# Kernel tuning notes

Measured on AMD Instinct MI355X. Metric: run time of the kernel, lower is better.

Reference implementation:

```python
import jax, jax.numpy as jnp
from jax import lax
import numpy as np

NUM_CLASSES = 80
SCORE_THR = 0.05
MIN_SIZE = 1.0
IOU_THR = 0.5
IMTOP = 100
PRE_NMS_K = 1000   # per-image candidate cap before NMS (jit-safe substitute for dynamic nonzero filtering)
N_IMG = 2
BBOX_CLIP = float(np.log(1000.0 / 16.0))  # standard dw/dh clamp in decode_boxes(clamp=True)


def setup_inputs() -> dict:
    key = jax.random.key(0)
    ks = jax.random.split(key, 12)
    R, C, S, CLIN = 2000, 256, 7, 1024
    c1 = C * S * S
    roi_maps = jax.random.normal(ks[0], (R, C, S, S), jnp.float32) * 0.1
    xy = jax.random.uniform(ks[1], (R, 2), jnp.float32, 0.0, 600.0)
    wh = jax.random.uniform(ks[2], (R, 2), jnp.float32, 8.0, 200.0)
    proposals = jnp.concatenate([xy, xy + wh], axis=-1)  # valid xyxy boxes
    imidx = jnp.sort(jax.random.randint(ks[3], (R,), 0, N_IMG)).astype(jnp.int32)
    imsizes = jnp.full((N_IMG, 2), 800.0, jnp.float32)  # (h, w) per image
    def lin(k, o, i):
        return jax.random.normal(k, (o, i), jnp.float32) * (1.0 / np.sqrt(i))
    return {
        'roi_maps': roi_maps, 'proposals': proposals, 'imidx': imidx, 'imsizes': imsizes,
        'fc1_w': lin(ks[4], CLIN, c1), 'fc1_b': jnp.zeros((CLIN,), jnp.float32),
        'fc2_w': lin(ks[5], CLIN, CLIN), 'fc2_b': jnp.zeros((CLIN,), jnp.float32),
        'cls_w': lin(ks[6], 1 + NUM_CLASSES, CLIN), 'cls_b': jnp.zeros((1 + NUM_CLASSES,), jnp.float32),
        'reg_w': lin(ks[7], NUM_CLASSES * 4, CLIN), 'reg_b': jnp.zeros((NUM_CLASSES * 4,), jnp.float32),
    }


def _nms_single(boxes, scores, cls):
    # boxes [K,4] xyxy (sorted by score desc), scores [K] (-1 = invalid), cls [K]
    K = scores.shape[0]
    valid = scores > 0.0
    # batched_nms trick: offset boxes by class so different classes never overlap
    off = cls.astype(boxes.dtype) * (jnp.max(boxes) + 1.0)
    ob = boxes + off[:, None]
    x1, y1, x2, y2 = ob[:, 0], ob[:, 1], ob[:, 2], ob[:, 3]
    area = (x2 - x1) * (y2 - y1)
    iw = jnp.clip(jnp.minimum(x2[:, None], x2[None, :]) - jnp.maximum(x1[:, None], x1[None, :]), 0.0)
    ih = jnp.clip(jnp.minimum(y2[:, None], y2[None, :]) - jnp.maximum(y1[:, None], y1[None, :]), 0.0)
    inter = iw * ih
    iou = inter / (area[:, None] + area[None, :] - inter + 1e-9)  # [K,K]
    ar = jnp.arange(K)

    def body(i, carry):
        sup, keep = carry
        k = jnp.logical_not(sup[i])
        keep = keep.at[i].set(k)
        sup = sup | (k & (iou[i] > IOU_THR) & (ar > i))
        return (sup, keep)

    sup, keep = lax.fori_loop(0, K, body, (jnp.logical_not(valid), jnp.zeros((K,), bool)))
    order = jnp.sort(jnp.where(keep, ar, K))[:IMTOP]
    vo = order < K
    idx = jnp.minimum(order, K - 1)
    b = jnp.where(vo[:, None], boxes[idx], 0.0)
    s = jnp.where(vo, scores[idx], 0.0)
    c = jnp.where(vo, cls[idx], -1)
    return b, s, c


def _forward(roi_maps, proposals, imsizes, fc1_w, fc1_b, fc2_w, fc2_b,
             cls_w, cls_b, reg_w, reg_b, imidx):
    R = roi_maps.shape[0]
    x = roi_maps.reshape(R, -1)
    x = jax.nn.relu(x @ fc1_w.T + fc1_b)
    x = jax.nn.relu(x @ fc2_w.T + fc2_b)
    reg = (x @ reg_w.T + reg_b).reshape(R, NUM_CLASSES, 4)  # per-class deltas
    logit = x @ cls_w.T + cls_b                              # [R, 1+C]
    scr = jax.nn.softmax(logit, axis=-1)[:, :-1]             # bckg_class_first=False -> drop last
    # convert_to_cwh
    pw = proposals[:, 2] - proposals[:, 0]
    ph = proposals[:, 3] - proposals[:, 1]
    pcx = proposals[:, 0] + 0.5 * pw
    pcy = proposals[:, 1] + 0.5 * ph
    # decode_boxes, mults=(0.1, 0.2), clamp dw/dh
    dx = reg[..., 0] * 0.1
    dy = reg[..., 1] * 0.1
    dw = jnp.minimum(reg[..., 2] * 0.2, BBOX_CLIP)
    dh = jnp.minimum(reg[..., 3] * 0.2, BBOX_CLIP)
    cx = dx * pw[:, None] + pcx[:, None]
    cy = dy * ph[:, None] + pcy[:, None]
    w = jnp.exp(dw) * pw[:, None]
    h = jnp.exp(dh) * ph[:, None]
    boxes = jnp.stack([cx - 0.5 * w, cy - 0.5 * h, cx + 0.5 * w, cy + 0.5 * h], axis=-1)  # [R,C,4]
    # clamp_to_canvas: imsizes is (h, w)
    sz = imsizes[imidx]  # [R,2]
    maxs = jnp.stack([sz[:, 1], sz[:, 0], sz[:, 1], sz[:, 0]], axis=-1)[:, None, :]
    boxes = jnp.clip(boxes, 0.0, maxs)
    bw = boxes[..., 2] - boxes[..., 0]
    bh = boxes[..., 3] - boxes[..., 1]
    # score_thr filter + remove_small, expressed as score masking (jit-safe)
    mask = (scr > SCORE_THR) & (bw >= MIN_SIZE) & (bh >= MIN_SIZE)
    scores = jnp.where(mask, scr, -1.0)  # [R,C]
    flat_boxes = boxes.reshape(-1, 4)
    flat_cls = jnp.broadcast_to(jnp.arange(NUM_CLASSES), (R, NUM_CLASSES)).reshape(-1)
    # per-image candidate scores, pre-NMS top-K
    img_mask = imidx[None, :] == jnp.arange(N_IMG)[:, None]            # [N,R]
    img_scores = jnp.where(img_mask[:, :, None], scores[None], -1.0).reshape(N_IMG, -1)
    top_s, top_i = lax.top_k(img_scores, PRE_NMS_K)                    # [N,K]
    b_k = flat_boxes[top_i]                                            # [N,K,4]
    c_k = flat_cls[top_i]                                              # [N,K]
    return jax.vmap(_nms_single)(b_k, top_s, c_k)


def reference(roi_maps, proposals, imidx, imsizes, fc1_w, fc1_b, fc2_w, fc2_b,
              cls_w, cls_b, reg_w, reg_b):
    return _forward(roi_maps, proposals, imsizes, fc1_w, fc1_b, fc2_w, fc2_b,
                    cls_w, cls_b, reg_w, reg_b, imidx)
```

## Files before the change

### kernel.cpp

```cpp
#include <hip/hip_runtime.h>
#include <cstdint>

typedef unsigned int u32;
typedef unsigned long long u64;
typedef _Float16 f16;
typedef f16 f16x8 __attribute__((ext_vector_type(8)));
typedef f16 f16x4 __attribute__((ext_vector_type(4)));
typedef float f32x4 __attribute__((ext_vector_type(4)));

#define R_ROIS 2000
#define CIN 12544
#define HID 1024
#define NCLS 80
#define NHEAD 401
#define RC (R_ROIS*NCLS)
#define KTOP 1000
#define IMTOP 100
#define KEY_NEG1 0x407FFFFFu
#define BBOX_CLIPV 4.135166556742356f
#define NCHUNK 157

__device__ __forceinline__ u32 fkey(float f) {
  u32 u = __float_as_uint(f);
  return (u & 0x80000000u) ? ~u : (u | 0x80000000u);
}
__device__ __forceinline__ float fkeyinv(u32 k) {
  u32 b = (k & 0x80000000u) ? (k & 0x7FFFFFFFu) : ~k;
  return __uint_as_float(b);
}
__device__ __forceinline__ u32 mkey(const u32* keys, const int* imidx, int i, int g) {
  int r = i / NCLS;
  return (imidx[r] == g) ? keys[i] : KEY_NEG1;
}

__device__ __forceinline__ void lds16(const f16* gsrc, f16* ldst) {
  __builtin_amdgcn_global_load_lds(
      (const __attribute__((address_space(1))) void*)gsrc,
      (__attribute__((address_space(3))) void*)ldst, 16, 0, 0);
}

__global__ __launch_bounds__(512, 4)
void gemm_f16x3(const f16* __restrict__ A1, const f16* __restrict__ A2,
                const f16* __restrict__ B1, const f16* __restrict__ B2,
                float* __restrict__ C, int M, int N, int K, int kLen)
{
  __shared__ __align__(16) f16 As1[2][128 * 32];
  __shared__ __align__(16) f16 As2[2][128 * 32];
  __shared__ __align__(16) f16 Bs1[2][128 * 32];
  __shared__ __align__(16) f16 Bs2[2][128 * 32];

  int gx = gridDim.x, gy = gridDim.y;
  int nblk = gx * gy * gridDim.z;
  int lid = blockIdx.x + gx * (blockIdx.y + gy * blockIdx.z);
  int cpx = nblk >> 3;
  int nlid = (lid & 7) * cpx + (lid >> 3);
  int bx = nlid % gx;
  int rem = nlid / gx;
  int by = rem % gy;
  int bz = rem / gy;

  int t = threadIdx.x;
  int w = t >> 6, lane = t & 63;
  int wm = w >> 2, wn = w & 3;
  int m0 = by * 128, n0 = bx * 128;
  int k0 = bz * kLen;
// ... 58 lines not shown
#pragma unroll
    for (int mi = 0; mi < 4; ++mi)
#pragma unroll
      for (int ni = 0; ni < 2; ++ni) {
        acc[mi][ni] = __builtin_amdgcn_mfma_f32_16x16x32_f16(af1[mi], bf1[ni], acc[mi][ni], 0, 0, 0);
        acc[mi][ni] = __builtin_amdgcn_mfma_f32_16x16x32_f16(af1[mi], bf2[ni], acc[mi][ni], 0, 0, 0);
        acc[mi][ni] = __builtin_amdgcn_mfma_f32_16x16x32_f16(af2[mi], bf1[ni], acc[mi][ni], 0, 0, 0);
      }
    __builtin_amdgcn_s_setprio(0);
    __builtin_amdgcn_sched_barrier(0);
    asm volatile("s_waitcnt vmcnt(0)" ::: "memory");
    __builtin_amdgcn_s_barrier();
    __builtin_amdgcn_sched_barrier(0);
    cur ^= 1;
  }

  int crow = m0 + wm * 64 + (lane >> 4) * 4;
  int ccol = n0 + wn * 32 + (lane & 15);
#pragma unroll
  for (int mi = 0; mi < 4; ++mi)
#pragma unroll
    for (int r = 0; r < 4; ++r) {
      int rm = crow + mi * 16 + r;
      if (rm < M) {
#pragma unroll
        for (int ni = 0; ni < 2; ++ni) {
          int cc = ccol + ni * 16;
          if (cc < N) atomicAdd(&C[(size_t)rm * N + cc], acc[mi][ni][r]);
        }
      }
    }
}

__global__ void split3_k(const float* __restrict__ s0, int c0,
                         const float* __restrict__ s1, int c1,
                         const float* __restrict__ s2, int c2,
                         f16* __restrict__ d0a, f16* __restrict__ d0b,
                         f16* __restrict__ d1a, f16* __restrict__ d1b,
                         f16* __restrict__ d2a, f16* __restrict__ d2b)
{
  int total = c0 + c1 + c2;
  for (int i = blockIdx.x * blockDim.x + threadIdx.x; i < total; i += gridDim.x * blockDim.x) {
    const float* src; f16 *da, *db; int j;
    if (i < c0) { src = s0; da = d0a; db = d0b; j = i; }
    else if (i < c0 + c1) { src = s1; da = d1a; db = d1b; j = i - c0; }
    else { src = s2; da = d2a; db = d2b; j = i - c0 - c1; }
    float4 v = ((const float4*)src)[j];
    f16x4 o1, o2;
    o1[0] = (f16)v.x; o2[0] = (f16)(v.x - (float)o1[0]);
    o1[1] = (f16)v.y; o2[1] = (f16)(v.y - (float)o1[1]);
    o1[2] = (f16)v.z; o2[2] = (f16)(v.z - (float)o1[2]);
    o1[3] = (f16)v.w; o2[3] = (f16)(v.w - (float)o1[3]);
    ((f16x4*)da)[j] = o1;
    ((f16x4*)db)[j] = o2;
  }
}

__global__ void packhead_k(const float* __restrict__ clsw, const float* __restrict__ regw,
                           f16* __restrict__ W1, f16* __restrict__ W2)
{
  int i = blockIdx.x * blockDim.x + threadIdx.x;
  if (i >= 512 * 256) return;
  int r = i >> 8, c4 = i & 255;
  int rr = (r < NHEAD) ? r : (NHEAD - 1);
  const float* src = (rr < 81) ? (clsw + (size_t)rr * HID) : (regw + (size_t)(rr - 81) * HID);
  float4 v = ((const float4*)src)[c4];
  f16x4 o1, o2;
  o1[0] = (f16)v.x; o2[0] = (f16)(v.x - (float)o1[0]);
  o1[1] = (f16)v.y; o2[1] = (f16)(v.y - (float)o1[1]);
  o1[2] = (f16)v.z; o2[2] = (f16)(v.z - (float)o1[2]);
  o1[3] = (f16)v.w; o2[3] = (f16)(v.w - (float)o1[3]);
  ((f16x4*)W1)[i] = o1;
  ((f16x4*)W2)[i] = o2;
}

__global__ void biasfill_k(const float* __restrict__ clsb, const float* __restrict__ regb,
                           float* __restrict__ H)
{
  int i = blockIdx.x * blockDim.x + threadIdx.x;
  if (i >= R_ROIS * NHEAD) return;
  int c = i % NHEAD;
  H[i] = (c < 81) ? clsb[c] : regb[c - 81];
}

__global__ void bias_relu_split_k(const float* __restrict__ X, const float* __restrict__ bias,
                                  f16* __restrict__ H1, f16* __restrict__ H2, int total)
{
  int i = blockIdx.x * blockDim.x + threadIdx.x;
  if (i >= total) return;
  float v = fmaxf(X[i] + bias[i & (HID - 1)], 0.f);
  f16 a = (f16)v;
  H1[i] = a;
  H2[i] = (f16)(v - (float)a);
}

__global__ __launch_bounds__(256, 2)
void gemm128(const float* __restrict__ A, int lda,
             const float* __restrict__ B, int ldb,
             float* __restrict__ C, int M, int N, int kLen)
{
  __shared__ float As[128][20];
  __shared__ float Bs[128][20];
  int t = threadIdx.x;
  int tx = t & 15, ty = t >> 4;
  int m0 = blockIdx.y * 128, n0 = blockIdx.x * 128;
  int k0 = blockIdx.z * kLen;
  float acc[8][8];
#pragma unroll
  for (int i = 0; i < 8; ++i)
#pragma unroll
    for (int j = 0; j < 8; ++j) acc[i][j] = 0.f;

  int lr = t >> 2;
  int lk = (t & 3) * 4;

  for (int ks = 0; ks < kLen; ks += 16) {
#pragma unroll
    for (int p = 0; p < 2; ++p) {
      int row = lr + p * 64;
      int rm = m0 + row; if (rm > M - 1) rm = M - 1;
      float4 av = *(const float4*)(A + (size_t)rm * lda + k0 + ks + lk);
      *(float4*)&As[row][lk] = av;
      int rn = n0 + row; if (rn > N - 1) rn = N - 1;
      float4 bv = *(const float4*)(B + (size_t)rn * ldb + k0 + ks + lk);
      *(float4*)&Bs[row][lk] = bv;
    }
    __syncthreads();
#pragma unroll
    for (int kk = 0; kk < 16; kk += 4) {
      float4 a4[8], b4[8];
#pragma unroll
      for (int i = 0; i < 8; ++i) a4[i] = *(const float4*)&As[ty + (i << 4)][kk];
#pragma unroll
      for (int j = 0; j < 8; ++j) b4[j] = *(const float4*)&Bs[tx + (j << 4)][kk];
#pragma unroll
      for (int i = 0; i < 8; ++i)
#pragma unroll
        for (int j = 0; j < 8; ++j) {
          acc[i][j] += a4[i].x * b4[j].x;
          acc[i][j] += a4[i].y * b4[j].y;
          acc[i][j] += a4[i].z * b4[j].z;
          acc[i][j] += a4[i].w * b4[j].w;
        }
    }
    __syncthreads();
  }
#pragma unroll
  for (int i = 0; i < 8; ++i) {
    int rm = m0 + ty + (i << 4);
    if (rm < M) {
#pragma unroll
      for (int j = 0; j < 8; ++j) {
        int rn = n0 + tx + (j << 4);
        atomicAdd(&C[(size_t)rm * N + rn], acc[i][j]);
      }
    }
  }
}

__global__ void bias_relu_k(float* __restrict__ X, const float* __restrict__ bias, int total4)
{
  int i4 = blockIdx.x * blockDim.x + threadIdx.x;
  if (i4 >= total4) return;
  int c4 = i4 & 255;
  float4 v = ((float4*)X)[i4];
  float4 b = ((const float4*)bias)[c4];
  v.x = fmaxf(v.x + b.x, 0.f);
  v.y = fmaxf(v.y + b.y, 0.f);
  v.z = fmaxf(v.z + b.z, 0.f);
  v.w = fmaxf(v.w + b.w, 0.f);
  ((float4*)X)[i4] = v;
}

__global__ __launch_bounds__(256)
void gemm_heads(const float* __restrict__ A,
                const float* __restrict__ clsw, const float* __restrict__ clsb,
                const float* __restrict__ regw, const float* __restrict__ regb,
                float* __restrict__ H)
{
  __shared__ float As[64][36];
  __shared__ float Bs[64][36];
  int t = threadIdx.x;
  int tx = t & 15, ty = t >> 4;
  int m0 = blockIdx.y * 64, n0 = blockIdx.x * 64;
  float acc[4][4] = {};
  int lr = t >> 3;
  int lk = (t & 7) * 4;

  for (int ks = 0; ks < HID; ks += 32) {
#pragma unroll
    for (int p = 0; p < 2; ++p) {
      int row = lr + p * 32;
      int rm = m0 + row; if (rm > R_ROIS - 1) rm = R_ROIS - 1;
      *(float4*)&As[row][lk] = *(const float4*)(A + (size_t)rm * HID + ks + lk);
      int rn = n0 + row; if (rn > NHEAD - 1) rn = NHEAD - 1;
      const float* bp = (rn < 81) ? (clsw + (size_t)rn * HID) : (regw + (size_t)(rn - 81) * HID);
      *(float4*)&Bs[row][lk] = *(const float4*)(bp + ks + lk);
    }
    __syncthreads();
#pragma unroll
    for (int kk = 0; kk < 32; kk += 4) {
      float4 a4[4], b4[4];
#pragma unroll
      for (int i = 0; i < 4; ++i) a4[i] = *(const float4*)&As[ty + (i << 4)][kk];
#pragma unroll
      for (int j = 0; j < 4; ++j) b4[j] = *(const float4*)&Bs[tx + (j << 4)][kk];
#pragma unroll
      for (int i = 0; i < 4; ++i)
#pragma unroll
        for (int j = 0; j < 4; ++j) {
          acc[i][j] += a4[i].x * b4[j].x;
          acc[i][j] += a4[i].y * b4[j].y;
          acc[i][j] += a4[i].z * b4[j].z;
          acc[i][j] += a4[i].w * b4[j].w;
        }
    }
    __syncthreads();
  }
#pragma unroll
  for (int i = 0; i < 4; ++i) {
    int rm = m0 + ty + (i << 4);
#pragma unroll
    for (int j = 0; j < 4; ++j) {
      int rn = n0 + tx + (j << 4);
      if (rm < R_ROIS && rn < NHEAD) {
        float b = (rn < 81) ? clsb[rn] : regb[rn - 81];
        H[(size_t)rm * NHEAD + rn] = acc[i][j] + b;
      }
    }
  }
}

__global__ __launch_bounds__(256)
void decode_k(const float* __restrict__ H, const float* __restrict__ prop,
              const int* __restrict__ imidx, const float* __restrict__ imsz,
              u32* __restrict__ keys, float* __restrict__ boxes)
{
  int lane = threadIdx.x & 63;
  int r = blockIdx.x * 4 + (threadIdx.x >> 6);
  const float* h = H + (size_t)r * NHEAD;
  float l0 = h[lane];
  float l1 = (lane < 17) ? h[64 + lane] : -1e30f;
  float mx = fmaxf(l0, l1);
#pragma unroll
  for (int o = 32; o; o >>= 1) mx = fmaxf(mx, __shfl_xor(mx, o));
  float e0 = expf(l0 - mx);
  float e1 = (lane < 17) ? expf(l1 - mx) : 0.f;
  float s = e0 + e1;
#pragma unroll
  for (int o = 32; o; o >>= 1) s += __shfl_xor(s, o);

  float px1 = prop[r * 4 + 0], py1 = prop[r * 4 + 1];
  float px2 = prop[r * 4 + 2], py2 = prop[r * 4 + 3];
  float pw = px2 - px1, ph = py2 - py1;
  float pcx = px1 + 0.5f * pw, pcy = py1 + 0.5f * ph;
  int g = imidx[r];
  float imh = imsz[g * 2 + 0], imw = imsz[g * 2 + 1];

#pragma unroll
  for (int q = 0; q < 2; ++q) {
    int c = (q == 0) ? lane : 64 + lane;
    bool on = (q == 0) ? true : (lane < 16);
    if (on) {
      float e = (q == 0) ? e0 : e1;
      float scr = e / s;
      const float* rg = h + 81 + c * 4;
      float dx = rg[0] * 0.1f, dy = rg[1] * 0.1f;
      float dw = fminf(rg[2] * 0.2f, BBOX_CLIPV);
      float dh = fminf(rg[3] * 0.2f, BBOX_CLIPV);
      float cx = dx * pw + pcx, cy = dy * ph + pcy;
      float w = expf(dw) * pw, hh = expf(dh) * ph;
      float x1 = cx - 0.5f * w, y1 = cy - 0.5f * hh;
      float x2 = cx + 0.5f * w, y2 = cy + 0.5f * hh;
      x1 = fminf(fmaxf(x1, 0.f), imw);
      x2 = fminf(fmaxf(x2, 0.f), imw);
      y1 = fminf(fmaxf(y1, 0.f), imh);
      y2 = fminf(fmaxf(y2, 0.f), imh);
      float bw = x2 - x1, bh = y2 - y1;
      bool msk = (scr > 0.05f) && (bw >= 1.f) && (bh >= 1.f);
      float sm = msk ? scr : -1.f;
      int idx = r * 80 + c;
      keys[idx] = fkey(sm);
      ((float4*)boxes)[idx] = make_float4(x1, y1, x2, y2);
    }
  }
}

__global__ void hist_k(const u32* __restrict__ keys, const int* __restrict__ imidx,
                       const u32* __restrict__ sel, u32* __restrict__ hist, int level, int nbins)
{
  __shared__ u32 lh[2048];
  int t = threadIdx.x, g = blockIdx.y;
  for (int b = t; b < 2048; b += 256) lh[b] = 0;
  __syncthreads();
  u32 b1 = 0, pre21 = 0;
  if (level == 2) b1 = sel[g * 8 + 0];
  if (level == 3) pre21 = (sel[g * 8 + 0] << 11) | sel[g * 8 + 1];
  for (int i = blockIdx.x * 256 + t; i < RC; i += gridDim.x * 256) {
    u32 k = mkey(keys, imidx, i, g);
    if (level == 1) atomicAdd(&lh[k >> 21], 1u);
    else if (level == 2) { if ((k >> 21) == b1) atomicAdd(&lh[(k >> 10) & 0x7FFu], 1u); }
    else { if ((k >> 10) == pre21) atomicAdd(&lh[k & 0x3FFu], 1u); }
  }
  __syncthreads();
  for (int b = t; b < nbins; b += 256) { u32 v = lh[b]; if (v) atomicAdd(&hist[g * nbins + b], v); }
}

__global__ void find_k(const u32* __restrict__ hist, int nbins, u32* __restrict__ sel, int level)
{
  __shared__ u32 sh[256];
  int t = threadIdx.x, g = blockIdx.x;
  int per = nbins >> 8;
  const u32* h = hist + g * nbins;
  u32 mySum = 0;
  for (int jj = 0; jj < per; ++jj) mySum += h[t * per + jj];
  u32 base = (level == 1) ? 0u : sel[g * 8 + 3];
  sh[t] = mySum; __syncthreads();
  for (int off = 1; off < 256; off <<= 1) {
    u32 v = (t + off < 256) ? sh[t + off] : 0u; __syncthreads();
    sh[t] += v; __syncthreads();
  }
  u32 c = base + ((t < 255) ? sh[t + 1] : 0u);
  for (int jj = per - 1; jj >= 0; --jj) {
    int b = t * per + jj;
    u32 cnt = h[b];
    if (c < KTOP && c + cnt >= KTOP) {
      if (level == 1) { sel[g * 8 + 0] = (u32)b; sel[g * 8 + 3] = c; }
      else if (level == 2) { sel[g * 8 + 1] = (u32)b; sel[g * 8 + 3] = c; }
      else {
        u32 T = (sel[g * 8 + 0] << 21) | (sel[g * 8 + 1] << 10) | (u32)b;
        sel[g * 8 + 4] = T; sel[g * 8 + 3] = c; sel[g * 8 + 5] = KTOP - c;
      }
    }
    c += cnt;
  }
}

__global__ void eqcount_k(const u32* __restrict__ keys, const int* __restrict__ imidx,
                          const u32* __restrict__ sel, u32* __restrict__ eqcnt)
{
  int g = blockIdx.y, t = threadIdx.x;
  int i = blockIdx.x * 1024 + t;
  u32 T = sel[g * 8 + 4];
  bool eq = (i < RC) && (mkey(keys, imidx, i, g) == T);
  u64 bal = __ballot(eq);
  __shared__ u32 wc[16];
  if ((t & 63) == 0) wc[t >> 6] = (u32)__popcll(bal);
  __syncthreads();
  if (t == 0) {
    u32 sum = 0;
    for (int w = 0; w < 16; ++w) sum += wc[w];
    eqcnt[g * 160 + blockIdx.x] = sum;
  }
}

__global__ void eqscan_k(const u32* __restrict__ eqcnt, u32* __restrict__ eqoff)
{
  __shared__ u32 sh[256];
  int t = threadIdx.x, g = blockIdx.x;
  u32 v = (t < NCHUNK) ? eqcnt[g * 160 + t] : 0u;
  sh[t] = v; __syncthreads();
  for (int off = 1; off < 256; off <<= 1) {
    u32 u = (t >= off) ? sh[t - off] : 0u; __syncthreads();
    sh[t] += u; __syncthreads();
  }
  if (t < NCHUNK) eqoff[g * 160 + t] = sh[t] - v;
}

__global__ void emit_k(const u32* __restrict__ keys, const int* __restrict__ imidx,
                       const u32* __restrict__ sel, const u32* __restrict__ eqoff,
                       u32* __restrict__ cntgt, u32* __restrict__ cand)
{
  int g = blockIdx.y, t = threadIdx.x;
  int i = blockIdx.x * 1024 + t;
  u32 T = sel[g * 8 + 4], m = sel[g * 8 + 5], ra = sel[g * 8 + 3];
  u32 k = (i < RC) ? mkey(keys, imidx, i, g) : 0u;
  if (k > T) { u32 p = atomicAdd(&cntgt[g], 1u); cand[g * 1024 + p] = (u32)i; }
  bool eq = (k == T);
  u64 bal = __ballot(eq);
  int w = t >> 6, lane = t & 63;
  __shared__ u32 wc[16];
  if (lane == 0) wc[w] = (u32)__popcll(bal);
  __syncthreads();
  u32 wb = 0;
  for (int x = 0; x < w; ++x) wb += wc[x];
  if (eq) {
    u32 lanePre = (u32)__popcll(bal & ((1ull << lane) - 1ull));
    u32 rank = eqoff[g * 160 + blockIdx.x] + wb + lanePre;
    if (rank < m) cand[g * 1024 + ra + rank] = (u32)i;
  }
}

__global__ __launch_bounds__(512)
void sort_k(const u32* __restrict__ cand, const u32* __restrict__ keys,
            const int* __restrict__ imidx, u64* __restrict__ sorted)
{
  __shared__ u64 sm[1024];
  int t = threadIdx.x, g = blockIdx.x;
#pragma unroll
  for (int p = 0; p < 2; ++p) {
    int s = t + p * 512;
    u64 e = ~0ull;
    if (s < KTOP) {
      u32 i = cand[g * 1024 + s];
      u32 k = mkey(keys, imidx, (int)i, g);
      e = ((u64)(~k) << 32) | (u64)i;
    }
    sm[s] = e;
  }
  __syncthreads();
  for (int kk = 2; kk <= 1024; kk <<= 1)
    for (int j = kk >> 1; j > 0; j >>= 1) {
#pragma unroll
      for (int p = 0; p < 2; ++p) {
        int i = t + p * 512;
        int ixj = i ^ j;
        if (ixj > i) {
          u64 a = sm[i], b = sm[ixj];
          bool up = ((i & kk) == 0);
          if ((a > b) == up) { sm[i] = b; sm[ixj] = a; }
        }
      }
      __syncthreads();
    }
  sorted[g * 1024 + t] = sm[t];
  sorted[g * 1024 + t + 512] = sm[t + 512];
}

__global__ void gather_k(const u64* __restrict__ sorted, const float* __restrict__ boxes,
                         u32* __restrict__ idx_k, float* __restrict__ sc_k,
                         float4* __restrict__ box_k, u64* __restrict__ inval,
                         float4* __restrict__ ob, float* __restrict__ area)
{
  __shared__ u32 smax;
  int t = threadIdx.x, g = blockIdx.x;
  if (t == 0) smax = 0;
  __syncthreads();
  u64 e = sorted[g * 1024 + t];
  u32 idx = (u32)e;
  u32 k = ~(u32)(e >> 32);
  float sc = fkeyinv(k);
  bool val = (t < KTOP) && (sc > 0.f);
  float4 b = make_float4(0.f, 0.f, 0.f, 0.f);
  if (t < KTOP) {
    idx_k[g * 1024 + t] = idx;
    sc_k[g * 1024 + t] = sc;
    b = ((const float4*)boxes)[idx];
    box_k[g * 1024 + t] = b;
    u32 m1 = __float_as_uint(b.x) > __float_as_uint(b.y) ? __float_as_uint(b.x) : __float_as_uint(b.y);
    u32 m2 = __float_as_uint(b.z) > __float_as_uint(b.w) ? __float_as_uint(b.z) : __float_as_uint(b.w);
    atomicMax(&smax, m1 > m2 ? m1 : m2);
  }
  u64 bal = __ballot(!val);
  if ((t & 63) == 0) inval[g * 16 + (t >> 6)] = bal;
  __syncthreads();
  float mx = __uint_as_float(smax);
  if (t < KTOP) {
    float off = (float)(idx % NCLS) * (mx + 1.0f);
    float4 o = make_float4(b.x + off, b.y + off, b.z + off, b.w + off);
    ob[g * 1024 + t] = o;
    area[g * 1024 + t] = (o.z - o.x) * (o.w - o.y);
  }
}

__global__ __launch_bounds__(256)
void nmsmat_k(const float4* __restrict__ ob, const float* __restrict__ area, u64* __restrict__ Mrow)
{
  __shared__ float4 sob[KTOP];
  __shared__ float sar[KTOP];
  int t = threadIdx.x, g = blockIdx.y;
  for (int s = t; s < KTOP; s += 256) { sob[s] = ob[g * 1024 + s]; sar[s] = area[g * 1024 + s]; }
  __syncthreads();
  int w = blockIdx.x * 256 + t;
  if (w >= KTOP * 16) return;
  int i = w >> 4, jw = w & 15;
  float4 bi = sob[i];
  float ai = sar[i];
  u64 bits = 0;
  int jbase = jw * 64;
  for (int b = 0; b < 64; ++b) {
    int j = jbase + b;
    if (j < KTOP && j > i) {
      float4 bj = sob[j];
      float iw = fminf(bi.z, bj.z) - fmaxf(bi.x, bj.x); iw = fmaxf(iw, 0.f);
      float ih = fminf(bi.w, bj.w) - fmaxf(bi.y, bj.y); ih = fmaxf(ih, 0.f);
      float inter = iw * ih;
      float iou = inter / (ai + sar[j] - inter + 1e-9f);
// ... 32 lines not shown
      sc = sc_k[g * 1024 + i];
      cf = (float)(idx_k[g * 1024 + i] % NCLS);
    }
    ((float4*)out)[g * IMTOP + s] = b;
    out[800 + g * IMTOP + s] = sc;
    out[1000 + g * IMTOP + s] = cf;
  }
}

extern "C" void kernel_launch(void* const* d_in, const int* in_sizes, int n_in,
                              void* d_out, int out_size, void* d_ws, size_t ws_size,
                              hipStream_t stream) {
  (void)in_sizes; (void)n_in; (void)out_size;
  const float* roi  = (const float*)d_in[0];
  const float* prop = (const float*)d_in[1];
  const int*   imix = (const int*)d_in[2];
  const float* imsz = (const float*)d_in[3];
  const float* fc1w = (const float*)d_in[4];
  const float* fc1b = (const float*)d_in[5];
  const float* fc2w = (const float*)d_in[6];
  const float* fc2b = (const float*)d_in[7];
  const float* clsw = (const float*)d_in[8];
  const float* clsb = (const float*)d_in[9];
  const float* regw = (const float*)d_in[10];
  const float* regb = (const float*)d_in[11];
  float* out = (float*)d_out;

  char* ws = (char*)d_ws;
  size_t o = 0;
  auto alloc = [&](size_t bytes) { size_t r = o; o += (bytes + 255) & ~(size_t)255; return r; };
  float* C1    = (float*)(ws + alloc((size_t)R_ROIS * HID * 4));
  float* C2    = (float*)(ws + alloc((size_t)R_ROIS * HID * 4));
  float* HEADS = (float*)(ws + alloc((size_t)R_ROIS * NHEAD * 4));
  u32*   KEYS  = (u32*)  (ws + alloc((size_t)RC * 4));
  float* BOXES = (float*)(ws + alloc((size_t)RC * 16));
  u64*   MROW  = (u64*)  (ws + alloc((size_t)2 * KTOP * 16 * 8));
  u64*   SORTED= (u64*)  (ws + alloc(2 * 1024 * 8));
  u32*   CAND  = (u32*)  (ws + alloc(2 * 1024 * 4));
  u32*   IDXK  = (u32*)  (ws + alloc(2 * 1024 * 4));
  float* SCK   = (float*)(ws + alloc(2 * 1024 * 4));
  float4* BOXK = (float4*)(ws + alloc(2 * 1024 * 16));
  float4* OBK  = (float4*)(ws + alloc(2 * 1024 * 16));
  float* AREA  = (float*)(ws + alloc(2 * 1024 * 4));
  u64*   INVAL = (u64*)  (ws + alloc(2 * 16 * 8));
  size_t zz0 = o;
  u32* HIST1 = (u32*)(ws + alloc(2 * 2048 * 4));
  u32* HIST2 = (u32*)(ws + alloc(2 * 2048 * 4));
  u32* HIST3 = (u32*)(ws + alloc(2 * 1024 * 4));
  u32* SEL   = (u32*)(ws + alloc(2 * 8 * 4));
  u32* CNTGT = (u32*)(ws + alloc(2 * 4));
  size_t zzBytes = o - zz0;
  u32* EQCNT = (u32*)(ws + alloc(2 * 160 * 4));
  u32* EQOFF = (u32*)(ws + alloc(2 * 160 * 4));

  f16* A1h = (f16*)(ws + alloc((size_t)R_ROIS * CIN * 2));
  f16* A2h = (f16*)(ws + alloc((size_t)R_ROIS * CIN * 2));
  f16* B1h = (f16*)(ws + alloc((size_t)HID * CIN * 2));
  f16* B2h = (f16*)(ws + alloc((size_t)HID * CIN * 2));
  f16* X1h = (f16*)(ws + alloc((size_t)R_ROIS * HID * 2));
  f16* X2h = (f16*)(ws + alloc((size_t)R_ROIS * HID * 2));
  f16* W1h = (f16*)(ws + alloc((size_t)HID * HID * 2));
  f16* W2h = (f16*)(ws + alloc((size_t)HID * HID * 2));
  f16* Y1h = (f16*)(ws + alloc((size_t)R_ROIS * HID * 2));
  f16* Y2h = (f16*)(ws + alloc((size_t)R_ROIS * HID * 2));
  f16* WH1 = (f16*)(ws + alloc((size_t)512 * HID * 2));
  f16* WH2 = (f16*)(ws + alloc((size_t)512 * HID * 2));
  bool fp16ok = (o <= ws_size);

  hipMemsetAsync(C1, 0, (size_t)2 * R_ROIS * HID * 4, stream);
  hipMemsetAsync(ws + zz0, 0, zzBytes, stream);

  if (fp16ok) {
    split3_k<<<2048, 256, 0, stream>>>(roi, R_ROIS * CIN / 4, fc1w, HID * CIN / 4,
                                       fc2w, HID * HID / 4,
                                       A1h, A2h, B1h, B2h, W1h, W2h);
    packhead_k<<<512, 256, 0, stream>>>(clsw, regw, WH1, WH2);
    biasfill_k<<<(R_ROIS * NHEAD + 255) / 256, 256, 0, stream>>>(clsb, regb, HEADS);
    gemm_f16x3<<<dim3(8, 16, 4), 512, 0, stream>>>(A1h, A2h, B1h, B2h, C1, R_ROIS, HID, CIN, 3136);
    bias_relu_split_k<<<(R_ROIS * HID + 255) / 256, 256, 0, stream>>>(C1, fc1b, X1h, X2h, R_ROIS * HID);
    gemm_f16x3<<<dim3(8, 16, 4), 512, 0, stream>>>(X1h, X2h, W1h, W2h, C2, R_ROIS, HID, HID, 256);
    bias_relu_split_k<<<(R_ROIS * HID + 255) / 256, 256, 0, stream>>>(C2, fc2b, Y1h, Y2h, R_ROIS * HID);
    gemm_f16x3<<<dim3(4, 16, 4), 512, 0, stream>>>(Y1h, Y2h, WH1, WH2, HEADS, R_ROIS, NHEAD, HID, 256);
  } else {
    gemm128<<<dim3(8, 16, 4), 256, 0, stream>>>(roi, CIN, fc1w, CIN, C1, R_ROIS, HID, 3136);
    bias_relu_k<<<2000, 256, 0, stream>>>(C1, fc1b, R_ROIS * HID / 4);
    gemm128<<<dim3(8, 16, 4), 256, 0, stream>>>(C1, HID, fc2w, HID, C2, R_ROIS, HID, 256);
    bias_relu_k<<<2000, 256, 0, stream>>>(C2, fc2b, R_ROIS * HID / 4);
    gemm_heads<<<dim3(7, 32), 256, 0, stream>>>(C2, clsw, clsb, regw, regb, HEADS);
  }
  decode_k<<<500, 256, 0, stream>>>(HEADS, prop, imix, imsz, KEYS, BOXES);
  hist_k<<<dim3(128, 2), 256, 0, stream>>>(KEYS, imix, SEL, HIST1, 1, 2048);
  find_k<<<2, 256, 0, stream>>>(HIST1, 2048, SEL, 1);
  hist_k<<<dim3(128, 2), 256, 0, stream>>>(KEYS, imix, SEL, HIST2, 2, 2048);
  find_k<<<2, 256, 0, stream>>>(HIST2, 2048, SEL, 2);
  hist_k<<<dim3(128, 2), 256, 0, stream>>>(KEYS, imix, SEL, HIST3, 3, 1024);
  find_k<<<2, 256, 0, stream>>>(HIST3, 1024, SEL, 3);
  eqcount_k<<<dim3(NCHUNK, 2), 1024, 0, stream>>>(KEYS, imix, SEL, EQCNT);
  eqscan_k<<<2, 256, 0, stream>>>(EQCNT, EQOFF);
  emit_k<<<dim3(NCHUNK, 2), 1024, 0, stream>>>(KEYS, imix, SEL, EQOFF, CNTGT, CAND);
  sort_k<<<2, 512, 0, stream>>>(CAND, KEYS, imix, SORTED);
  gather_k<<<2, 1024, 0, stream>>>(SORTED, BOXES, IDXK, SCK, BOXK, INVAL, OBK, AREA);
  nmsmat_k<<<dim3(63, 2), 256, 0, stream>>>(OBK, AREA, MROW);
  nmsscan_k<<<2, 64, 0, stream>>>(MROW, INVAL, IDXK, SCK, BOXK, out);
}
```

Baseline: 634.0 us.

## Fuse top-k selection pipeline into single per-image kernel and merge prep kernels

Replaces the chain of histogram, find, eqcount, scan, emit, sort and gather kernels with one select_k block per image. That block runs the three radix passes, candidate emission and the bitonic sort in shared memory, and decode now writes per-image key arrays. The three preprocessing kernels are merged into one prep_k, and bias_relu_split is vectorised to float4. This removes about a dozen small launches and a memset, but the selection now runs on only two blocks, each scanning 160K keys three times, so per-block serial work grows.

```diff
diff --git a/kernel.cpp b/kernel.cpp
--- a/kernel.cpp
+++ b/kernel.cpp
@@ -18,7 +18,6 @@
 #define IMTOP 100
 #define KEY_NEG1 0x407FFFFFu
 #define BBOX_CLIPV 4.135166556742356f
-#define NCHUNK 157
 
 __device__ __forceinline__ u32 fkey(float f) {
   u32 u = __float_as_uint(f);
@@ -27,10 +26,6 @@
 __device__ __forceinline__ float fkeyinv(u32 k) {
   u32 b = (k & 0x80000000u) ? (k & 0x7FFFFFFFu) : ~k;
   return __uint_as_float(b);
-}
-__device__ __forceinline__ u32 mkey(const u32* keys, const int* imidx, int i, int g) {
-  int r = i / NCLS;
-  return (imidx[r] == g) ? keys[i] : KEY_NEG1;
 }
 
 __device__ __forceinline__ void lds16(const f16* gsrc, f16* ldst) {
@@ -155,66 +150,70 @@
     }
 }
 
-__global__ void split3_k(const float* __restrict__ s0, int c0,
-                         const float* __restrict__ s1, int c1,
-                         const float* __restrict__ s2, int c2,
-                         f16* __restrict__ d0a, f16* __restrict__ d0b,
-                         f16* __restrict__ d1a, f16* __restrict__ d1b,
-                         f16* __restrict__ d2a, f16* __restrict__ d2b)
-{
-  int total = c0 + c1 + c2;
-  for (int i = blockIdx.x * blockDim.x + threadIdx.x; i < total; i += gridDim.x * blockDim.x) {
-    const float* src; f16 *da, *db; int j;
-    if (i < c0) { src = s0; da = d0a; db = d0b; j = i; }
-    else if (i < c0 + c1) { src = s1; da = d1a; db = d1b; j = i - c0; }
-    else { src = s2; da = d2a; db = d2b; j = i - c0 - c1; }
-    float4 v = ((const float4*)src)[j];
-    f16x4 o1, o2;
-    o1[0] = (f16)v.x; o2[0] = (f16)(v.x - (float)o1[0]);
-    o1[1] = (f16)v.y; o2[1] = (f16)(v.y - (float)o1[1]);
-    o1[2] = (f16)v.z; o2[2] = (f16)(v.z - (float)o1[2]);
-    o1[3] = (f16)v.w; o2[3] = (f16)(v.w - (float)o1[3]);
-    ((f16x4*)da)[j] = o1;
-    ((f16x4*)db)[j] = o2;
-  }
-}
-
-__global__ void packhead_k(const float* __restrict__ clsw, const float* __restrict__ regw,
-                           f16* __restrict__ W1, f16* __restrict__ W2)
-{
-  int i = blockIdx.x * blockDim.x + threadIdx.x;
-  if (i >= 512 * 256) return;
-  int r = i >> 8, c4 = i & 255;
-  int rr = (r < NHEAD) ? r : (NHEAD - 1);
-  const float* src = (rr < 81) ? (clsw + (size_t)rr * HID) : (regw + (size_t)(rr - 81) * HID);
-  float4 v = ((const float4*)src)[c4];
-  f16x4 o1, o2;
+__device__ __forceinline__ void split4(float4 v, f16x4& o1, f16x4& o2) {
   o1[0] = (f16)v.x; o2[0] = (f16)(v.x - (float)o1[0]);
   o1[1] = (f16)v.y; o2[1] = (f16)(v.y - (float)o1[1]);
   o1[2] = (f16)v.z; o2[2] = (f16)(v.z - (float)o1[2]);
   o1[3] = (f16)v.w; o2[3] = (f16)(v.w - (float)o1[3]);
-  ((f16x4*)W1)[i] = o1;
-  ((f16x4*)W2)[i] = o2;
-}
-
-__global__ void biasfill_k(const float* __restrict__ clsb, const float* __restrict__ regb,
-                           float* __restrict__ H)
-{
-  int i = blockIdx.x * blockDim.x + threadIdx.x;
-  if (i >= R_ROIS * NHEAD) return;
-  int c = i % NHEAD;
-  H[i] = (c < 81) ? clsb[c] : regb[c - 81];
+}
+
+__global__ void prep_k(const float* __restrict__ roi, const float* __restrict__ fc1w,
+                       const float* __restrict__ fc2w, const float* __restrict__ clsw,
+                       const float* __restrict__ regw, const float* __restrict__ clsb,
+                       const float* __restrict__ regb,
+                       f16* __restrict__ A1h, f16* __restrict__ A2h,
+                       f16* __restrict__ B1h, f16* __restrict__ B2h,
+                       f16* __restrict__ W1h, f16* __restrict__ W2h,
+                       f16* __restrict__ WH1, f16* __restrict__ WH2,
+                       float* __restrict__ HEADS)
+{
+  const int c0 = R_ROIS * CIN / 4;
+  const int c1 = HID * CIN / 4;
+  const int c2 = HID * HID / 4;
+  const int c3 = 512 * 256;
+  const int c4 = R_ROIS * NHEAD;
+  const int e0 = c0, e1 = e0 + c1, e2 = e1 + c2, e3 = e2 + c3, e4 = e3 + c4;
+  for (int i = blockIdx.x * blockDim.x + threadIdx.x; i < e4; i += gridDim.x * blockDim.x) {
+    f16x4 o1, o2;
+    if (i < e0) {
+      split4(((const float4*)roi)[i], o1, o2);
+      ((f16x4*)A1h)[i] = o1; ((f16x4*)A2h)[i] = o2;
+    } else if (i < e1) {
+      int j = i - e0;
+      split4(((const float4*)fc1w)[j], o1, o2);
+      ((f16x4*)B1h)[j] = o1; ((f16x4*)B2h)[j] = o2;
+    } else if (i < e2) {
+      int j = i - e1;
+      split4(((const float4*)fc2w)[j], o1, o2);
+      ((f16x4*)W1h)[j] = o1; ((f16x4*)W2h)[j] = o2;
+    } else if (i < e3) {
+      int j = i - e2;
+      int r = j >> 8, c4i = j & 255;
+      int rr = (r < NHEAD) ? r : (NHEAD - 1);
+      const float* src = (rr < 81) ? (clsw + (size_t)rr * HID) : (regw + (size_t)(rr - 81) * HID);
+      split4(((const float4*)src)[c4i], o1, o2);
+      ((f16x4*)WH1)[j] = o1; ((f16x4*)WH2)[j] = o2;
+    } else {
+      int j = i - e3;
+      int c = j % NHEAD;
+      HEADS[j] = (c < 81) ? clsb[c] : regb[c - 81];
+    }
+  }
 }
 
 __global__ void bias_relu_split_k(const float* __restrict__ X, const float* __restrict__ bias,
-                                  f16* __restrict__ H1, f16* __restrict__ H2, int total)
-{
-  int i = blockIdx.x * blockDim.x + threadIdx.x;
-  if (i >= total) return;
-  float v = fmaxf(X[i] + bias[i & (HID - 1)], 0.f);
-  f16 a = (f16)v;
-  H1[i] = a;
-  H2[i] = (f16)(v - (float)a);
+                                  f16* __restrict__ H1, f16* __restrict__ H2, int total4)
+{
+  int i4 = blockIdx.x * blockDim.x + threadIdx.x;
+  if (i4 >= total4) return;
+  float4 v = ((const float4*)X)[i4];
+  float4 b = ((const float4*)bias)[i4 & 255];
+  v.x = fmaxf(v.x + b.x, 0.f); v.y = fmaxf(v.y + b.y, 0.f);
+  v.z = fmaxf(v.z + b.z, 0.f); v.w = fmaxf(v.w + b.w, 0.f);
+  f16x4 o1, o2;
+  split4(v, o1, o2);
+  ((f16x4*)H1)[i4] = o1;
+  ((f16x4*)H2)[i4] = o2;
 }
 
 __global__ __launch_bounds__(256, 2)
@@ -233,20 +232,16 @@
   for (int i = 0; i < 8; ++i)
 #pragma unroll
     for (int j = 0; j < 8; ++j) acc[i][j] = 0.f;
-
   int lr = t >> 2;
   int lk = (t & 3) * 4;
-
   for (int ks = 0; ks < kLen; ks += 16) {
 #pragma unroll
     for (int p = 0; p < 2; ++p) {
       int row = lr + p * 64;
       int rm = m0 + row; if (rm > M - 1) rm = M - 1;
-      float4 av = *(const float4*)(A + (size_t)rm * lda + k0 + ks + lk);
-      *(float4*)&As[row][lk] = av;
+      *(float4*)&As[row][lk] = *(const float4*)(A + (size_t)rm * lda + k0 + ks + lk);
       int rn = n0 + row; if (rn > N - 1) rn = N - 1;
-      float4 bv = *(const float4*)(B + (size_t)rn * ldb + k0 + ks + lk);
-      *(float4*)&Bs[row][lk] = bv;
+      *(float4*)&Bs[row][lk] = *(const float4*)(B + (size_t)rn * ldb + k0 + ks + lk);
     }
     __syncthreads();
 #pragma unroll
@@ -273,10 +268,8 @@
     int rm = m0 + ty + (i << 4);
     if (rm < M) {
 #pragma unroll
-      for (int j = 0; j < 8; ++j) {
-        int rn = n0 + tx + (j << 4);
-        atomicAdd(&C[(size_t)rm * N + rn], acc[i][j]);
-      }
+      for (int j = 0; j < 8; ++j)
+        atomicAdd(&C[(size_t)rm * N + n0 + tx + (j << 4)], acc[i][j]);
     }
   }
 }
@@ -285,13 +278,10 @@
 {
   int i4 = blockIdx.x * blockDim.x + threadIdx.x;
   if (i4 >= total4) return;
-  int c4 = i4 & 255;
   float4 v = ((float4*)X)[i4];
-  float4 b = ((const float4*)bias)[c4];
-  v.x = fmaxf(v.x + b.x, 0.f);
-  v.y = fmaxf(v.y + b.y, 0.f);
-  v.z = fmaxf(v.z + b.z, 0.f);
-  v.w = fmaxf(v.w + b.w, 0.f);
+  float4 b = ((const float4*)bias)[i4 & 255];
+  v.x = fmaxf(v.x + b.x, 0.f); v.y = fmaxf(v.y + b.y, 0.f);
+  v.z = fmaxf(v.z + b.z, 0.f); v.w = fmaxf(v.w + b.w, 0.f);
   ((float4*)X)[i4] = v;
 }
 
@@ -309,7 +299,6 @@
   float acc[4][4] = {};
   int lr = t >> 3;
   int lk = (t & 7) * 4;
-
   for (int ks = 0; ks < HID; ks += 32) {
 #pragma unroll
     for (int p = 0; p < 2; ++p) {
@@ -357,7 +346,7 @@
 __global__ __launch_bounds__(256)
 void decode_k(const float* __restrict__ H, const float* __restrict__ prop,
               const int* __restrict__ imidx, const float* __restrict__ imsz,
-              u32* __restrict__ keys, float* __restrict__ boxes)
+              u32* __restrict__ keys0, u32* __restrict__ keys1, float* __restrict__ boxes)
 {
   int lane = threadIdx.x & 63;
   int r = blockIdx.x * 4 + (threadIdx.x >> 6);
@@ -401,168 +390,155 @@
       y2 = fminf(fmaxf(y2, 0.f), imh);
       float bw = x2 - x1, bh = y2 - y1;
       bool msk = (scr > 0.05f) && (bw >= 1.f) && (bh >= 1.f);
-      float sm = msk ? scr : -1.f;
+      u32 kk = fkey(msk ? scr : -1.f);
       int idx = r * 80 + c;
-      keys[idx] = fkey(sm);
+      keys0[idx] = (g == 0) ? kk : KEY_NEG1;
+      keys1[idx] = (g == 1) ? kk : KEY_NEG1;
       ((float4*)boxes)[idx] = make_float4(x1, y1, x2, y2);
     }
   }
 }
 
-__global__ void hist_k(const u32* __restrict__ keys, const int* __restrict__ imidx,
-                       const u32* __restrict__ sel, u32* __restrict__ hist, int level, int nbins)
+__global__ __launch_bounds__(1024)
+void select_k(const u32* __restrict__ keys0, const u32* __restrict__ keys1,
+              const float* __restrict__ boxes,
+              u32* __restrict__ idx_k, float* __restrict__ sc_k,
+              float4* __restrict__ box_k, u64* __restrict__ inval,
+              float4* __restrict__ ob, float* __restrict__ area)
 {
   __shared__ u32 lh[2048];
-  int t = threadIdx.x, g = blockIdx.y;
-  for (int b = t; b < 2048; b += 256) lh[b] = 0;
-  __syncthreads();
-  u32 b1 = 0, pre21 = 0;
-  if (level == 2) b1 = sel[g * 8 + 0];
-  if (level == 3) pre21 = (sel[g * 8 + 0] << 11) | sel[g * 8 + 1];
-  for (int i = blockIdx.x * 256 + t; i < RC; i += gridDim.x * 256) {
-    u32 k = mkey(keys, imidx, i, g);
-    if (level == 1) atomicAdd(&lh[k >> 21], 1u);
-    else if (level == 2) { if ((k >> 21) == b1) atomicAdd(&lh[(k >> 10) & 0x7FFu], 1u); }
-    else { if ((k >> 10) == pre21) atomicAdd(&lh[k & 0x3FFu], 1u); }
-  }
-  __syncthreads();
-  for (int b = t; b < nbins; b += 256) { u32 v = lh[b]; if (v) atomicAdd(&hist[g * nbins + b], v); }
-}
-
-__global__ void find_k(const u32* __restrict__ hist, int nbins, u32* __restrict__ sel, int level)
-{
-  __shared__ u32 sh[256];
-  int t = threadIdx.x, g = blockIdx.x;
-  int per = nbins >> 8;
-  const u32* h = hist + g * nbins;
-  u32 mySum = 0;
-  for (int jj = 0; jj < per; ++jj) mySum += h[t * per + jj];
-  u32 base = (level == 1) ? 0u : sel[g * 8 + 3];
-  sh[t] = mySum; __syncthreads();
-  for (int off = 1; off < 256; off <<= 1) {
-    u32 v = (t + off < 256) ? sh[t + off] : 0u; __syncthreads();
-    sh[t] += v; __syncthreads();
-  }
-  u32 c = base + ((t < 255) ? sh[t + 1] : 0u);
-  for (int jj = per - 1; jj >= 0; --jj) {
-    int b = t * per + jj;
-    u32 cnt = h[b];
+  __shared__ u32 sh[1024];
+  __shared__ u32 candL[1024];
+  __shared__ u64 sm[1024];
+  __shared__ u32 selS[8];
+  __shared__ u32 wc[16];
+  __shared__ u32 gtCnt, eqBase, smax;
+
+  int g = blockIdx.x, t = threadIdx.x;
+  int w = t >> 6, lane = t & 63;
+  const u32* keys = g ? keys1 : keys0;
+
+  lh[t] = 0; lh[t + 1024] = 0;
+  __syncthreads();
+  for (int i = t; i < RC; i += 1024) atomicAdd(&lh[keys[i] >> 21], 1u);
+  __syncthreads();
+  {
+    sh[t] = lh[2 * t] + lh[2 * t + 1];
+    __syncthreads();
+    for (int off = 1; off < 1024; off <<= 1) {
+      u32 v = (t + off < 1024) ? sh[t + off] : 0u; __syncthreads();
+      sh[t] += v; __syncthreads();
+    }
+    u32 c = (t < 1023) ? sh[t + 1] : 0u;
+    for (int jj = 1; jj >= 0; --jj) {
+      int b = 2 * t + jj;
+      u32 cnt = lh[b];
+      if (c < KTOP && c + cnt >= KTOP) { selS[0] = (u32)b; selS[2] = c; }
+      c += cnt;
+    }
+  }
+  __syncthreads();
+  u32 b1 = selS[0];
+  lh[t] = 0; lh[t + 1024] = 0;
+  __syncthreads();
+  for (int i = t; i < RC; i += 1024) {
+    u32 k = keys[i];
+    if ((k >> 21) == b1) atomicAdd(&lh[(k >> 10) & 0x7FFu], 1u);
+  }
+  __syncthreads();
+  {
+    u32 base = selS[2];
+    sh[t] = lh[2 * t] + lh[2 * t + 1];
+    __syncthreads();
+    for (int off = 1; off < 1024; off <<= 1) {
+      u32 v = (t + off < 1024) ? sh[t + off] : 0u; __syncthreads();
+      sh[t] += v; __syncthreads();
+    }
+    u32 c = base + ((t < 1023) ? sh[t + 1] : 0u);
+    for (int jj = 1; jj >= 0; --jj) {
+      int b = 2 * t + jj;
+      u32 cnt = lh[b];
+      if (c < KTOP && c + cnt >= KTOP) { selS[1] = (u32)b; selS[3] = c; }
+      c += cnt;
+    }
+  }
+  __syncthreads();
+  u32 pre21 = (b1 << 11) | selS[1];
+  lh[t] = 0;
+  __syncthreads();
+  for (int i = t; i < RC; i += 1024) {
+    u32 k = keys[i];
+    if ((k >> 10) == pre21) atomicAdd(&lh[k & 0x3FFu], 1u);
+  }
+  __syncthreads();
+  {
+    u32 base = selS[3];
+    sh[t] = lh[t];
+    __syncthreads();
+    for (int off = 1; off < 1024; off <<= 1) {
+      u32 v = (t + off < 1024) ? sh[t + off] : 0u; __syncthreads();
+      sh[t] += v; __syncthreads();
+    }
+    u32 c = base + ((t < 1023) ? sh[t + 1] : 0u);
+    u32 cnt = lh[t];
     if (c < KTOP && c + cnt >= KTOP) {
-      if (level == 1) { sel[g * 8 + 0] = (u32)b; sel[g * 8 + 3] = c; }
-      else if (level == 2) { sel[g * 8 + 1] = (u32)b; sel[g * 8 + 3] = c; }
-      else {
-        u32 T = (sel[g * 8 + 0] << 21) | (sel[g * 8 + 1] << 10) | (u32)b;
-        sel[g * 8 + 4] = T; sel[g * 8 + 3] = c; sel[g * 8 + 5] = KTOP - c;
-      }
-    }
-    c += cnt;
-  }
-}
-
-__global__ void eqcount_k(const u32* __restrict__ keys, const int* __restrict__ imidx,
-                          const u32* __restrict__ sel, u32* __restrict__ eqcnt)
-{
-  int g = blockIdx.y, t = threadIdx.x;
-  int i = blockIdx.x * 1024 + t;
-  u32 T = sel[g * 8 + 4];
-  bool eq = (i < RC) && (mkey(keys, imidx, i, g) == T);
-  u64 bal = __ballot(eq);
-  __shared__ u32 wc[16];
-  if ((t & 63) == 0) wc[t >> 6] = (u32)__popcll(bal);
-  __syncthreads();
-  if (t == 0) {
-    u32 sum = 0;
-    for (int w = 0; w < 16; ++w) sum += wc[w];
-    eqcnt[g * 160 + blockIdx.x] = sum;
-  }
-}
-
-__global__ void eqscan_k(const u32* __restrict__ eqcnt, u32* __restrict__ eqoff)
-{
-  __shared__ u32 sh[256];
-  int t = threadIdx.x, g = blockIdx.x;
-  u32 v = (t < NCHUNK) ? eqcnt[g * 160 + t] : 0u;
-  sh[t] = v; __syncthreads();
-  for (int off = 1; off < 256; off <<= 1) {
-    u32 u = (t >= off) ? sh[t - off] : 0u; __syncthreads();
-    sh[t] += u; __syncthreads();
-  }
-  if (t < NCHUNK) eqoff[g * 160 + t] = sh[t] - v;
-}
-
-__global__ void emit_k(const u32* __restrict__ keys, const int* __restrict__ imidx,
-                       const u32* __restrict__ sel, const u32* __restrict__ eqoff,
-                       u32* __restrict__ cntgt, u32* __restrict__ cand)
-{
-  int g = blockIdx.y, t = threadIdx.x;
-  int i = blockIdx.x * 1024 + t;
-  u32 T = sel[g * 8 + 4], m = sel[g * 8 + 5], ra = sel[g * 8 + 3];
-  u32 k = (i < RC) ? mkey(keys, imidx, i, g) : 0u;
-  if (k > T) { u32 p = atomicAdd(&cntgt[g], 1u); cand[g * 1024 + p] = (u32)i; }
-  bool eq = (k == T);
-  u64 bal = __ballot(eq);
-  int w = t >> 6, lane = t & 63;
-  __shared__ u32 wc[16];
-  if (lane == 0) wc[w] = (u32)__popcll(bal);
-  __syncthreads();
-  u32 wb = 0;
-  for (int x = 0; x < w; ++x) wb += wc[x];
-  if (eq) {
-    u32 lanePre = (u32)__popcll(bal & ((1ull << lane) - 1ull));
-    u32 rank = eqoff[g * 160 + blockIdx.x] + wb + lanePre;
-    if (rank < m) cand[g * 1024 + ra + rank] = (u32)i;
-  }
-}
-
-__global__ __launch_bounds__(512)
-void sort_k(const u32* __restrict__ cand, const u32* __restrict__ keys,
-            const int* __restrict__ imidx, u64* __restrict__ sorted)
-{
-  __shared__ u64 sm[1024];
-  int t = threadIdx.x, g = blockIdx.x;
-#pragma unroll
-  for (int p = 0; p < 2; ++p) {
-    int s = t + p * 512;
+      selS[4] = (pre21 << 10) | (u32)t;
+      selS[6] = c;
+      selS[5] = KTOP - c;
+    }
+  }
+  __syncthreads();
+  u32 T = selS[4], mm = selS[5], cGT = selS[6];
+
+  if (t == 0) { gtCnt = 0; eqBase = 0; }
+  __syncthreads();
+  for (int c0 = 0; c0 < RC; c0 += 1024) {
+    int i = c0 + t;
+    bool inr = (i < RC);
+    u32 k = inr ? keys[i] : 0u;
+    if (inr && k > T) { u32 p = atomicAdd(&gtCnt, 1u); candL[p] = (u32)i; }
+    bool eq = inr && (k == T);
+    u64 bal = __ballot(eq);
+    if (lane == 0) wc[w] = (u32)__popcll(bal);
+    __syncthreads();
+    u32 pre = 0, tot = 0;
+#pragma unroll
+    for (int x = 0; x < 16; ++x) { u32 v = wc[x]; if (x < w) pre += v; tot += v; }
+    if (eq) {
+      u32 rank = eqBase + pre + (u32)__popcll(bal & ((1ull << lane) - 1ull));
+      if (rank < mm) candL[cGT + rank] = (u32)i;
+    }
+    __syncthreads();
+    if (t == 0) eqBase += tot;
+    __syncthreads();
+  }
+
+  {
     u64 e = ~0ull;
-    if (s < KTOP) {
-      u32 i = cand[g * 1024 + s];
-      u32 k = mkey(keys, imidx, (int)i, g);
-      e = ((u64)(~k) << 32) | (u64)i;
-    }
-    sm[s] = e;
-  }
-  __syncthreads();
-  for (int kk = 2; kk <= 1024; kk <<= 1)
-    for (int j = kk >> 1; j > 0; j >>= 1) {
-#pragma unroll
-      for (int p = 0; p < 2; ++p) {
-        int i = t + p * 512;
-        int ixj = i ^ j;
-        if (ixj > i) {
-          u64 a = sm[i], b = sm[ixj];
-          bool up = ((i & kk) == 0);
-          if ((a > b) == up) { sm[i] = b; sm[ixj] = a; }
-        }
+    if (t < KTOP) {
+      u32 i = candL[t];
+      e = ((u64)(~keys[i]) << 32) | (u64)i;
+    }
+    sm[t] = e;
+  }
+  __syncthreads();
+  for (int kk2 = 2; kk2 <= 1024; kk2 <<= 1)
+    for (int j = kk2 >> 1; j > 0; j >>= 1) {
+      int ixj = t ^ j;
+      if (ixj > t) {
+        u64 a = sm[t], b = sm[ixj];
+        bool up = ((t & kk2) == 0);
+        if ((a > b) == up) { sm[t] = b; sm[ixj] = a; }
       }
       __syncthreads();
     }
-  sorted[g * 1024 + t] = sm[t];
-  sorted[g * 1024 + t + 512] = sm[t + 512];
-}
-
-__global__ void gather_k(const u64* __restrict__ sorted, const float* __restrict__ boxes,
-                         u32* __restrict__ idx_k, float* __restrict__ sc_k,
-                         float4* __restrict__ box_k, u64* __restrict__ inval,
-                         float4* __restrict__ ob, float* __restrict__ area)
-{
-  __shared__ u32 smax;
-  int t = threadIdx.x, g = blockIdx.x;
+
   if (t == 0) smax = 0;
   __syncthreads();
-  u64 e = sorted[g * 1024 + t];
+  u64 e = sm[t];
   u32 idx = (u32)e;
-  u32 k = ~(u32)(e >> 32);
-  float sc = fkeyinv(k);
+  u32 k2 = ~(u32)(e >> 32);
+  float sc = fkeyinv(k2);
   bool val = (t < KTOP) && (sc > 0.f);
   float4 b = make_float4(0.f, 0.f, 0.f, 0.f);
   if (t < KTOP) {
@@ -575,7 +551,7 @@
     atomicMax(&smax, m1 > m2 ? m1 : m2);
   }
   u64 bal = __ballot(!val);
-  if ((t & 63) == 0) inval[g * 16 + (t >> 6)] = bal;
+  if (lane == 0) inval[g * 16 + w] = bal;
   __syncthreads();
   float mx = __uint_as_float(smax);
   if (t < KTOP) {
@@ -674,26 +650,16 @@
   float* C1    = (float*)(ws + alloc((size_t)R_ROIS * HID * 4));
   float* C2    = (float*)(ws + alloc((size_t)R_ROIS * HID * 4));
   float* HEADS = (float*)(ws + alloc((size_t)R_ROIS * NHEAD * 4));
-  u32*   KEYS  = (u32*)  (ws + alloc((size_t)RC * 4));
+  u32*   KEYS0 = (u32*)  (ws + alloc((size_t)RC * 4));
+  u32*   KEYS1 = (u32*)  (ws + alloc((size_t)RC * 4));
   float* BOXES = (float*)(ws + alloc((size_t)RC * 16));
   u64*   MROW  = (u64*)  (ws + alloc((size_t)2 * KTOP * 16 * 8));
-  u64*   SORTED= (u64*)  (ws + alloc(2 * 1024 * 8));
-  u32*   CAND  = (u32*)  (ws + alloc(2 * 1024 * 4));
   u32*   IDXK  = (u32*)  (ws + alloc(2 * 1024 * 4));
   float* SCK   = (float*)(ws + alloc(2 * 1024 * 4));
   float4* BOXK = (float4*)(ws + alloc(2 * 1024 * 16));
   float4* OBK  = (float4*)(ws + alloc(2 * 1024 * 16));
   float* AREA  = (float*)(ws + alloc(2 * 1024 * 4));
   u64*   INVAL = (u64*)  (ws + alloc(2 * 16 * 8));
-  size_t zz0 = o;
-  u32* HIST1 = (u32*)(ws + alloc(2 * 2048 * 4));
-  u32* HIST2 = (u32*)(ws + alloc(2 * 2048 * 4));
-  u32* HIST3 = (u32*)(ws + alloc(2 * 1024 * 4));
-  u32* SEL   = (u32*)(ws + alloc(2 * 8 * 4));
-  u32* CNTGT = (u32*)(ws + alloc(2 * 4));
-  size_t zzBytes = o - zz0;
-  u32* EQCNT = (u32*)(ws + alloc(2 * 160 * 4));
-  u32* EQOFF = (u32*)(ws + alloc(2 * 160 * 4));
 
   f16* A1h = (f16*)(ws + alloc((size_t)R_ROIS * CIN * 2));
   f16* A2h = (f16*)(ws + alloc((size_t)R_ROIS * CIN * 2));
@@ -710,18 +676,14 @@
   bool fp16ok = (o <= ws_size);
 
   hipMemsetAsync(C1, 0, (size_t)2 * R_ROIS * HID * 4, stream);
-  hipMemsetAsync(ws + zz0, 0, zzBytes, stream);
 
   if (fp16ok) {
-    split3_k<<<2048, 256, 0, stream>>>(roi, R_ROIS * CIN / 4, fc1w, HID * CIN / 4,
-                                       fc2w, HID * HID / 4,
-                                       A1h, A2h, B1h, B2h, W1h, W2h);
-    packhead_k<<<512, 256, 0, stream>>>(clsw, regw, WH1, WH2);
-    biasfill_k<<<(R_ROIS * NHEAD + 255) / 256, 256, 0, stream>>>(clsb, regb, HEADS);
+    prep_k<<<2048, 256, 0, stream>>>(roi, fc1w, fc2w, clsw, regw, clsb, regb,
+                                     A1h, A2h, B1h, B2h, W1h, W2h, WH1, WH2, HEADS);
     gemm_f16x3<<<dim3(8, 16, 4), 512, 0, stream>>>(A1h, A2h, B1h, B2h, C1, R_ROIS, HID, CIN, 3136);
-    bias_relu_split_k<<<(R_ROIS * HID + 255) / 256, 256, 0, stream>>>(C1, fc1b, X1h, X2h, R_ROIS * HID);
+    bias_relu_split_k<<<(R_ROIS * HID / 4 + 255) / 256, 256, 0, stream>>>(C1, fc1b, X1h, X2h, R_ROIS * HID / 4);
     gemm_f16x3<<<dim3(8, 16, 4), 512, 0, stream>>>(X1h, X2h, W1h, W2h, C2, R_ROIS, HID, HID, 256);
-    bias_relu_split_k<<<(R_ROIS * HID + 255) / 256, 256, 0, stream>>>(C2, fc2b, Y1h, Y2h, R_ROIS * HID);
+    bias_relu_split_k<<<(R_ROIS * HID / 4 + 255) / 256, 256, 0, stream>>>(C2, fc2b, Y1h, Y2h, R_ROIS * HID / 4);
     gemm_f16x3<<<dim3(4, 16, 4), 512, 0, stream>>>(Y1h, Y2h, WH1, WH2, HEADS, R_ROIS, NHEAD, HID, 256);
   } else {
     gemm128<<<dim3(8, 16, 4), 256, 0, stream>>>(roi, CIN, fc1w, CIN, C1, R_ROIS, HID, 3136);
@@ -730,18 +692,8 @@
     bias_relu_k<<<2000, 256, 0, stream>>>(C2, fc2b, R_ROIS * HID / 4);
     gemm_heads<<<dim3(7, 32), 256, 0, stream>>>(C2, clsw, clsb, regw, regb, HEADS);
   }
-  decode_k<<<500, 256, 0, stream>>>(HEADS, prop, imix, imsz, KEYS, BOXES);
-  hist_k<<<dim3(128, 2), 256, 0, stream>>>(KEYS, imix, SEL, HIST1, 1, 2048);
-  find_k<<<2, 256, 0, stream>>>(HIST1, 2048, SEL, 1);
-  hist_k<<<dim3(128, 2), 256, 0, stream>>>(KEYS, imix, SEL, HIST2, 2, 2048);
-  find_k<<<2, 256, 0, stream>>>(HIST2, 2048, SEL, 2);
-  hist_k<<<dim3(128, 2), 256, 0, stream>>>(KEYS, imix, SEL, HIST3, 3, 1024);
-  find_k<<<2, 256, 0, stream>>>(HIST3, 1024, SEL, 3);
-  eqcount_k<<<dim3(NCHUNK, 2), 1024, 0, stream>>>(KEYS, imix, SEL, EQCNT);
-  eqscan_k<<<2, 256, 0, stream>>>(EQCNT, EQOFF);
-  emit_k<<<dim3(NCHUNK, 2), 1024, 0, stream>>>(KEYS, imix, SEL, EQOFF, CNTGT, CAND);
-  sort_k<<<2, 512, 0, stream>>>(CAND, KEYS, imix, SORTED);
-  gather_k<<<2, 1024, 0, stream>>>(SORTED, BOXES, IDXK, SCK, BOXK, INVAL, OBK, AREA);
+  decode_k<<<500, 256, 0, stream>>>(HEADS, prop, imix, imsz, KEYS0, KEYS1, BOXES);
+  select_k<<<2, 1024, 0, stream>>>(KEYS0, KEYS1, BOXES, IDXK, SCK, BOXK, INVAL, OBK, AREA);
   nmsmat_k<<<dim3(63, 2), 256, 0, stream>>>(OBK, AREA, MROW);
   nmsscan_k<<<2, 64, 0, stream>>>(MROW, INVAL, IDXK, SCK, BOXK, out);
 }
```

Result: slower. 1.084 ms (+71.0%).
